# Optimization experiments

Hardware: AMD Instinct MI355X
Metric: run time of the kernel (lower is better)

Reference implementation:

```python
import jax, jax.numpy as jnp
import numpy as np
import math

HEADS = 16
D_MODEL = 1024
D_K = D_MODEL // HEADS


def setup_inputs() -> dict:
    key = jax.random.key(0)
    ks = jax.random.split(key, 11)
    B, S = 2, 2048
    s = 1.0 / math.sqrt(D_MODEL)
    return {
        "q": jax.random.normal(ks[0], (B, S, D_MODEL), jnp.float32),
        "k": jax.random.normal(ks[1], (B, S, D_MODEL), jnp.float32),
        "v": jax.random.normal(ks[2], (B, S, D_MODEL), jnp.float32),
        "Wq": jax.random.normal(ks[3], (D_MODEL, D_MODEL), jnp.float32) * s,
        "bq": jax.random.normal(ks[4], (D_MODEL,), jnp.float32) * s,
        "Wk": jax.random.normal(ks[5], (D_MODEL, D_MODEL), jnp.float32) * s,
        "bk": jax.random.normal(ks[6], (D_MODEL,), jnp.float32) * s,
        "Wv": jax.random.normal(ks[7], (D_MODEL, D_MODEL), jnp.float32) * s,
        "bv": jax.random.normal(ks[8], (D_MODEL,), jnp.float32) * s,
        "Wo": jax.random.normal(ks[9], (D_MODEL, D_MODEL), jnp.float32) * s,
        "bo": jax.random.normal(ks[10], (D_MODEL,), jnp.float32) * s,
    }


def reference(q, k, v, Wq, bq, Wk, bk, Wv, bv, Wo, bo):
    B, S, _ = q.shape
    # linear projections, split heads: [B, H, S, d_k]
    def proj(x, W, b):
        y = x @ W.T + b
        return y.reshape(B, -1, HEADS, D_K).transpose(0, 2, 1, 3)
    qh, kh, vh = proj(q, Wq, bq), proj(k, Wk, bk), proj(v, Wv, bv)
    # abs-modified scaled dot-product attention (no mask, eval -> no dropout)
    scores = jnp.abs(jnp.einsum("bhsd,bhtd->bhst", qh, kh) / math.sqrt(D_K))
    attn = jax.nn.softmax(scores, axis=-1)
    out = jnp.einsum("bhst,bhtd->bhsd", attn, vh)
    concat = out.transpose(0, 2, 1, 3).reshape(B, S, D_MODEL)
    return concat @ Wo.T + bo
```

## Files before the change

kernel.cpp:

```cpp
#include <hip/hip_runtime.h>

#define HEADS 16
#define DK 64
#define DM 1024
#define SEQ 2048
#define BATCH 2

using bf16x8 = __attribute__((ext_vector_type(8))) short;
using short4v = __attribute__((ext_vector_type(4))) short;
using f32x4 = __attribute__((ext_vector_type(4))) float;

static __device__ __forceinline__ short f2bf(float x) {
  union { float f; unsigned u; } c;
  c.f = x;
  unsigned r = (c.u + 0x7FFFu + ((c.u >> 16) & 1u)) >> 16;
  return (short)r;
}

static __device__ __forceinline__ void gload_lds16(const void* g, void* l) {
  __builtin_amdgcn_global_load_lds(
      (const __attribute__((address_space(1))) void*)g,
      (__attribute__((address_space(3))) void*)l, 16, 0, 0);
}

__global__ __launch_bounds__(256) void cvt7(
    const float* __restrict__ s0, const float* __restrict__ s1,
    const float* __restrict__ s2, const float* __restrict__ s3,
    const float* __restrict__ s4, const float* __restrict__ s5,
    const float* __restrict__ s6, short* d0, short* d1, short* d2, short* d3,
    short* d4, short* d5, short* d6) {
  const int y = blockIdx.y;
  const float* s;
  short* d;
  int n;
  switch (y) {
    case 0: s = s0; d = d0; n = BATCH * SEQ * DM; break;
    case 1: s = s1; d = d1; n = BATCH * SEQ * DM; break;
    case 2: s = s2; d = d2; n = BATCH * SEQ * DM; break;
    case 3: s = s3; d = d3; n = DM * DM; break;
    case 4: s = s4; d = d4; n = DM * DM; break;
    case 5: s = s5; d = d5; n = DM * DM; break;
    default: s = s6; d = d6; n = DM * DM; break;
  }
  const int n4 = n >> 2;
  const int stride = gridDim.x * 256;
  for (int i = blockIdx.x * 256 + threadIdx.x; i < n4; i += stride) {
    float4 v = ((const float4*)s)[i];
    short4v o;
    o.x = f2bf(v.x);
    o.y = f2bf(v.y);
    o.z = f2bf(v.z);
    o.w = f2bf(v.w);
    ((short4v*)d)[i] = o;
  }
}

__global__ __launch_bounds__(256) void proj_qkv(
    const short* __restrict__ Aq, const short* __restrict__ Ak,
    const short* __restrict__ Av, const short* __restrict__ Wq_,
    const short* __restrict__ Wk_, const short* __restrict__ Wv_,
    const float* __restrict__ bq, const float* __restrict__ bk,
    const float* __restrict__ bv, short* __restrict__ Qh,
    short* __restrict__ Kh, short* __restrict__ Vt) {
  __shared__ short smem[128 * 136];
  short* As = smem;
  short* Ws = smem + 8192;

  const int z = blockIdx.z;
  const short* A = z == 0 ? Aq : z == 1 ? Ak : Av;
  const short* W = z == 0 ? Wq_ : z == 1 ? Wk_ : Wv_;
  const float* bias = z == 0 ? bq : z == 1 ? bk : bv;
  short* C = z == 0 ? Qh : z == 1 ? Kh : Vt;
  const bool tr = (z == 2);

  const int tid = threadIdx.x;
  const int wave = tid >> 6, lane = tid & 63;
  const int quad = lane >> 4, l15 = lane & 15;
  const int n0 = blockIdx.x * 128, m0 = blockIdx.y * 128;
  const int mh = (wave & 1) * 64, nh = (wave >> 1) * 64;
  const int ldr = lane >> 3, ldc = lane & 7;

  f32x4 acc[4][4] = {};

  for (int k0 = 0; k0 < 1024; k0 += 64) {
    __syncthreads();
#pragma unroll
    for (int i = 0; i < 8; ++i) {
      int seg = wave * 8 + i;
      int r = (seg & 15) * 8 + ldr;
      int kb = ldc ^ (r & 7);
      if (seg < 16)
        gload_lds16(&A[(size_t)(m0 + r) * 1024 + k0 + kb * 8], &As[seg * 512]);
      else
        gload_lds16(&W[(size_t)(n0 + r) * 1024 + k0 + kb * 8],
                    &Ws[(seg - 16) * 512]);
    }
    __syncthreads();
#pragma unroll
    for (int ks = 0; ks < 2; ++ks) {
      bf16x8 a[4], b[4];
      int kb = ks * 4 + quad;
#pragma unroll
      for (int f = 0; f < 4; ++f) {
        int rm = mh + f * 16 + l15;
        int rn = nh + f * 16 + l15;
        a[f] = *(const bf16x8*)&As[rm * 64 + (kb ^ (rm & 7)) * 8];
        b[f] = *(const bf16x8*)&Ws[rn * 64 + (kb ^ (rn & 7)) * 8];
      }
#pragma unroll
      for (int mf = 0; mf < 4; ++mf)
#pragma unroll
        for (int nf = 0; nf < 4; ++nf)
          acc[mf][nf] = __builtin_amdgcn_mfma_f32_16x16x32_bf16(
              a[mf], b[nf], acc[mf][nf], 0, 0, 0);
    }
  }

  float bvv[4];
#pragma unroll
  for (int nf = 0; nf < 4; ++nf) bvv[nf] = bias[n0 + nh + nf * 16 + l15];

  __syncthreads();
  short* Cb = smem;

  if (!tr) {
#pragma unroll
    for (int mf = 0; mf < 4; ++mf)
#pragma unroll
      for (int nf = 0; nf < 4; ++nf)
#pragma unroll
        for (int r = 0; r < 4; ++r)
          Cb[(mh + mf * 16 + quad * 4 + r) * 136 + nh + nf * 16 + l15] =
              f2bf(acc[mf][nf][r] + bvv[nf]);
    __syncthreads();
#pragma unroll
    for (int j = 0; j < 8; ++j) {
      int cid = tid + 256 * j;
      int row = cid >> 4, cb = cid & 15;
      bf16x8 v = *(const bf16x8*)&Cb[row * 136 + cb * 8];
      int m = m0 + row, n = n0 + cb * 8;
      int b = m >> 11, s = m & (SEQ - 1), h = n >> 6, d = n & 63;
      *(bf16x8*)&C[((size_t)(b * HEADS + h) * SEQ + s) * DK + d] = v;
    }
  } else {
#pragma unroll
    for (int mf = 0; mf < 4; ++mf)
#pragma unroll
      for (int nf = 0; nf < 4; ++nf) {
        short4v p;
        p.x = f2bf(acc[mf][nf][0] + bvv[nf]);
        p.y = f2bf(acc[mf][nf][1] + bvv[nf]);
        p.z = f2bf(acc[mf][nf][2] + bvv[nf]);
        p.w = f2bf(acc[mf][nf][3] + bvv[nf]);
        *(short4v*)&Cb[(nh + nf * 16 + l15) * 136 + mh + mf * 16 + quad * 4] =
            p;
      }
    __syncthreads();
#pragma unroll
    for (int j = 0; j < 8; ++j) {
      int cid = tid + 256 * j;
      int row = cid >> 4, cb = cid & 15;
      bf16x8 v = *(const bf16x8*)&Cb[row * 136 + cb * 8];
      int n = n0 + row, m = m0 + cb * 8;
      int b = m >> 11, s = m & (SEQ - 1), h = n >> 6, d = n & 63;
      *(bf16x8*)&C[((size_t)(b * HEADS + h) * DK + d) * SEQ + s] = v;
    }
  }
}

__global__ __launch_bounds__(256) void proj_out(const short* __restrict__ A,
                                                const short* __restrict__ W,
                                                const float* __restrict__ bias,
                                                float* __restrict__ C) {
  __shared__ short smem[128 * 136];
  short* As = smem;
  short* Ws = smem + 8192;

  const int tid = threadIdx.x;
  const int wave = tid >> 6, lane = tid & 63;
  const int quad = lane >> 4, l15 = lane & 15;
  const int n0 = blockIdx.x * 128, m0 = blockIdx.y * 128;
  const int mh = (wave & 1) * 64, nh = (wave >> 1) * 64;
  const int ldr = lane >> 3, ldc = lane & 7;

  f32x4 acc[4][4] = {};

  for (int k0 = 0; k0 < 1024; k0 += 64) {
    __syncthreads();
#pragma unroll
    for (int i = 0; i < 8; ++i) {
      int seg = wave * 8 + i;
      int r = (seg & 15) * 8 + ldr;
      int kb = ldc ^ (r & 7);
      if (seg < 16)
        gload_lds16(&A[(size_t)(m0 + r) * 1024 + k0 + kb * 8], &As[seg * 512]);
      else
        gload_lds16(&W[(size_t)(n0 + r) * 1024 + k0 + kb * 8],
                    &Ws[(seg - 16) * 512]);
    }
    __syncthreads();
#pragma unroll
    for (int ks = 0; ks < 2; ++ks) {
      bf16x8 a[4], b[4];
      int kb = ks * 4 + quad;
#pragma unroll
      for (int f = 0; f < 4; ++f) {
        int rm = mh + f * 16 + l15;
        int rn = nh + f * 16 + l15;
        a[f] = *(const bf16x8*)&As[rm * 64 + (kb ^ (rm & 7)) * 8];
        b[f] = *(const bf16x8*)&Ws[rn * 64 + (kb ^ (rn & 7)) * 8];
      }
#pragma unroll
      for (int mf = 0; mf < 4; ++mf)
#pragma unroll
        for (int nf = 0; nf < 4; ++nf)
          acc[mf][nf] = __builtin_amdgcn_mfma_f32_16x16x32_bf16(
              a[mf], b[nf], acc[mf][nf], 0, 0, 0);
    }
  }

  float bvv[4];
#pragma unroll
  for (int nf = 0; nf < 4; ++nf) bvv[nf] = bias[n0 + nh + nf * 16 + l15];
#pragma unroll
  for (int mf = 0; mf < 4; ++mf)
#pragma unroll
    for (int nf = 0; nf < 4; ++nf)
#pragma unroll
      for (int r = 0; r < 4; ++r)
        C[(size_t)(m0 + mh + mf * 16 + quad * 4 + r) * 1024 + n0 + nh +
          nf * 16 + l15] = acc[mf][nf][r] + bvv[nf];
}

__global__ __launch_bounds__(256) void attn_mfma(const short* __restrict__ Qh,
                                                 const short* __restrict__ Kh,
                                                 const short* __restrict__ VtG,
                                                 short* __restrict__ concat) {
  __shared__ short Ks[64 * 64];
  __shared__ short Vt[64 * 64];
  __shared__ short Ps[128 * 64];

  const int tid = threadIdx.x;
  const int wave = tid >> 6, lane = tid & 63;
  const int quad = lane >> 4, l15 = lane & 15;
  const int bh = blockIdx.y;
  const int q0 = blockIdx.x * 128;
  const size_t base = (size_t)bh * SEQ * DK;
  const int ldr = lane >> 3, ldc = lane & 7;

  bf16x8 qf[2][2];
#pragma unroll
  for (int mf = 0; mf < 2; ++mf)
#pragma unroll
    for (int ks = 0; ks < 2; ++ks)
      qf[mf][ks] =
          *(const bf16x8*)&Qh[base +
                              (size_t)(q0 + wave * 32 + mf * 16 + l15) * 64 +
                              ks * 32 + quad * 8];

  f32x4 O[2][4] = {};
  float lsum[2][4] = {};

  for (int kt = 0; kt < SEQ / 64; ++kt) {
    __syncthreads();
#pragma unroll
    for (int i = 0; i < 2; ++i) {
      int seg = wave * 2 + i;
      int row = seg * 8 + ldr;
      int kb = ldc ^ (row & 7);
      gload_lds16(&Kh[base + (size_t)(kt * 64 + row) * 64 + kb * 8],
                  &Ks[seg * 512]);
      gload_lds16(&VtG[base + (size_t)row * SEQ + kt * 64 + kb * 8],
                  &Vt[seg * 512]);
    }
    __syncthreads();

    f32x4 sf[2][4] = {};
#pragma unroll
    for (int ks = 0; ks < 2; ++ks) {
      bf16x8 bfr[4];
      int kb = ks * 4 + quad;
#pragma unroll
      for (int nf = 0; nf < 4; ++nf) {
        int n = nf * 16 + l15;
        bfr[nf] = *(const bf16x8*)&Ks[n * 64 + (kb ^ (n & 7)) * 8];
      }
#pragma unroll
      for (int mf = 0; mf < 2; ++mf)
#pragma unroll
        for (int nf = 0; nf < 4; ++nf)
          sf[mf][nf] = __builtin_amdgcn_mfma_f32_16x16x32_bf16(
              qf[mf][ks], bfr[nf], sf[mf][nf], 0, 0, 0);
    }

    const int h2 = l15 >> 3, lo3 = l15 & 7;
#pragma unroll
    for (int mf = 0; mf < 2; ++mf)
#pragma unroll
      for (int nf = 0; nf < 4; ++nf) {
        const int ch = 2 * nf + h2;
#pragma unroll
        for (int r = 0; r < 4; ++r) {
          float e = __expf(fabsf(sf[mf][nf][r]) * 0.125f);
          lsum[mf][r] += e;
          int row = wave * 32 + mf * 16 + quad * 4 + r;
          Ps[(row << 6) + ((ch ^ ((row >> 1) & 7)) << 3) + lo3] = f2bf(e);
        }
      }
    __threadfence_block();

#pragma unroll
    for (int ks = 0; ks < 2; ++ks) {
      bf16x8 av[2], bvv[4];
      int kb = ks * 4 + quad;
#pragma unroll
      for (int mf = 0; mf < 2; ++mf) {
        int row = wave * 32 + mf * 16 + l15;
        av[mf] = *(const bf16x8*)&Ps[(row << 6) +
                                     ((kb ^ ((row >> 1) & 7)) << 3)];
      }
#pragma unroll
      for (int nf = 0; nf < 4; ++nf) {
        int n = nf * 16 + l15;
        bvv[nf] = *(const bf16x8*)&Vt[n * 64 + (kb ^ (n & 7)) * 8];
      }
#pragma unroll
      for (int mf = 0; mf < 2; ++mf)
#pragma unroll
        for (int nf = 0; nf < 4; ++nf)
          O[mf][nf] = __builtin_amdgcn_mfma_f32_16x16x32_bf16(
              av[mf], bvv[nf], O[mf][nf], 0, 0, 0);
    }
  }

  float inv[2][4];
#pragma unroll
  for (int mf = 0; mf < 2; ++mf)
#pragma unroll
    for (int r = 0; r < 4; ++r) {
      float s = lsum[mf][r];
#pragma unroll
      for (int x = 1; x < 16; x <<= 1) s += __shfl_xor(s, x, 64);
      inv[mf][r] = 1.f / s;
    }

  __syncthreads();
  const int h2 = l15 >> 3, lo3 = l15 & 7;
#pragma unroll
  for (int mf = 0; mf < 2; ++mf)
#pragma unroll
    for (int nf = 0; nf < 4; ++nf) {
      const int ch = 2 * nf + h2;
#pragma unroll
      for (int r = 0; r < 4; ++r) {
        int row = wave * 32 + mf * 16 + quad * 4 + r;
        Ps[(row << 6) + ((ch ^ ((row >> 1) & 7)) << 3) + lo3] =
            f2bf(O[mf][nf][r] * inv[mf][r]);
      }
    }
  __syncthreads();
  const int b = bh >> 4, h = bh & 15;
#pragma unroll
  for (int j = 0; j < 4; ++j) {
    int cid = tid + 256 * j;
    int row = cid >> 3, cb = cid & 7;
    bf16x8 v = *(const bf16x8*)&Ps[(row << 6) + ((cb ^ ((row >> 1) & 7)) << 3)];
    *(bf16x8*)&concat[((size_t)(b * SEQ + q0 + row)) * DM + h * 64 + cb * 8] =
        v;
  }
}

extern "C" void kernel_launch(void* const* d_in, const int* in_sizes, int n_in,
                              void* d_out, int out_size, void* d_ws,
                              size_t ws_size, hipStream_t stream) {
  const float* q = (const float*)d_in[0];
  const float* k = (const float*)d_in[1];
  const float* v = (const float*)d_in[2];
  const float* Wq = (const float*)d_in[3];
  const float* bq = (const float*)d_in[4];
  const float* Wk = (const float*)d_in[5];
  const float* bk = (const float*)d_in[6];
  const float* Wv = (const float*)d_in[7];
  const float* bv = (const float*)d_in[8];
  const float* Wo = (const float*)d_in[9];
  const float* bo = (const float*)d_in[10];

  short* ws = (short*)d_ws;
  const size_t T4 = (size_t)BATCH * SEQ * DM;
  const size_t T1 = (size_t)DM * DM;
  short* qb = ws;
  short* kb_ = ws + T4;
  short* vb = ws + 2 * T4;
  short* Wqb = ws + 3 * T4;
  short* Wkb = Wqb + T1;
  short* Wvb = Wqb + 2 * T1;
  short* Wob = Wqb + 3 * T1;
  short* Qh = Wqb + 4 * T1;
  short* Kh = Qh + T4;
  short* VtG = Qh + 2 * T4;
  short* cc = Qh + 3 * T4;

  cvt7<<<dim3(1024, 7), 256, 0, stream>>>(q, k, v, Wq, Wk, Wv, Wo, qb, kb_, vb,
                                          Wqb, Wkb, Wvb, Wob);

  proj_qkv<<<dim3(DM / 128, (BATCH * SEQ) / 128, 3), 256, 0, stream>>>(
      qb, kb_, vb, Wqb, Wkb, Wvb, bq, bk, bv, Qh, Kh, VtG);

  attn_mfma<<<dim3(SEQ / 128, BATCH * HEADS), 256, 0, stream>>>(Qh, Kh, VtG,
                                                                cc);

  proj_out<<<dim3(DM / 128, (BATCH * SEQ) / 128), 256, 0, stream>>>(
      cc, Wob, bo, (float*)d_out);
}
```

Measured before the change: 244.6 us.

## Double-buffer K/V tiles, fold softmax scale into Q, compute row sums via MFMA

The attention kernel now prefetches the next K/V tile into a second LDS buffer while computing on the current one, which removes one barrier per iteration. It shrinks the query tile to 64 rows (one 16-row fragment per wave), doubling the grid size. The scores are computed transposed (K as the A operand), so each lane writes packed 4-element P rows. The 1/sqrt(d_k)*log2(e) scale is folded into the Q projection epilogue, so the loop can use exp2 directly. Row sums come from an extra MFMA against a ones vector instead of per-element adds and a final shuffle reduction, at the cost of more MFMA work per tile and less Q reuse of each loaded K/V tile.

```diff
diff --git a/kernel.cpp b/kernel.cpp
--- a/kernel.cpp
+++ b/kernel.cpp
@@ -124,6 +124,7 @@
   short* Cb = smem;
 
   if (!tr) {
+    const float osc = (z == 0) ? 0.18033688011112042f : 1.0f;
 #pragma unroll
     for (int mf = 0; mf < 4; ++mf)
 #pragma unroll
@@ -131,7 +132,7 @@
 #pragma unroll
         for (int r = 0; r < 4; ++r)
           Cb[(mh + mf * 16 + quad * 4 + r) * 136 + nh + nf * 16 + l15] =
-              f2bf(acc[mf][nf][r] + bvv[nf]);
+              f2bf((acc[mf][nf][r] + bvv[nf]) * osc);
     __syncthreads();
 #pragma unroll
     for (int j = 0; j < 8; ++j) {
@@ -236,136 +237,128 @@
                                                  const short* __restrict__ Kh,
                                                  const short* __restrict__ VtG,
                                                  short* __restrict__ concat) {
-  __shared__ short Ks[64 * 64];
-  __shared__ short Vt[64 * 64];
-  __shared__ short Ps[128 * 64];
+  __shared__ short Ksm[2][64 * 64];
+  __shared__ short Vsm[2][64 * 64];
+  __shared__ short Ps[64 * 64];
 
   const int tid = threadIdx.x;
   const int wave = tid >> 6, lane = tid & 63;
   const int quad = lane >> 4, l15 = lane & 15;
   const int bh = blockIdx.y;
-  const int q0 = blockIdx.x * 128;
+  const int q0 = blockIdx.x * 64;
   const size_t base = (size_t)bh * SEQ * DK;
   const int ldr = lane >> 3, ldc = lane & 7;
-
-  bf16x8 qf[2][2];
-#pragma unroll
-  for (int mf = 0; mf < 2; ++mf)
-#pragma unroll
-    for (int ks = 0; ks < 2; ++ks)
-      qf[mf][ks] =
-          *(const bf16x8*)&Qh[base +
-                              (size_t)(q0 + wave * 32 + mf * 16 + l15) * 64 +
-                              ks * 32 + quad * 8];
-
-  f32x4 O[2][4] = {};
-  float lsum[2][4] = {};
-
+  const int row = wave * 16 + l15;
+  const int rsw = (row & 7) << 1;
+
+  bf16x8 qf[2];
+#pragma unroll
+  for (int ks = 0; ks < 2; ++ks)
+    qf[ks] =
+        *(const bf16x8*)&Qh[base + (size_t)(q0 + row) * 64 + ks * 32 + quad * 8];
+
+  bf16x8 ones;
+#pragma unroll
+  for (int i = 0; i < 8; ++i) ones[i] = (short)0x3F80;
+
+  f32x4 O[4] = {};
+  f32x4 Lacc = {};
+
+#pragma unroll
+  for (int i = 0; i < 2; ++i) {
+    int seg = wave * 2 + i;
+    int r = seg * 8 + ldr;
+    int kb = ldc ^ (r & 7);
+    gload_lds16(&Kh[base + (size_t)r * 64 + kb * 8], &Ksm[0][seg * 512]);
+    gload_lds16(&VtG[base + (size_t)r * SEQ + kb * 8], &Vsm[0][seg * 512]);
+  }
+  __syncthreads();
+
+  int cur = 0;
   for (int kt = 0; kt < SEQ / 64; ++kt) {
-    __syncthreads();
-#pragma unroll
-    for (int i = 0; i < 2; ++i) {
-      int seg = wave * 2 + i;
-      int row = seg * 8 + ldr;
-      int kb = ldc ^ (row & 7);
-      gload_lds16(&Kh[base + (size_t)(kt * 64 + row) * 64 + kb * 8],
-                  &Ks[seg * 512]);
-      gload_lds16(&VtG[base + (size_t)row * SEQ + kt * 64 + kb * 8],
-                  &Vt[seg * 512]);
-    }
-    __syncthreads();
-
-    f32x4 sf[2][4] = {};
+    if (kt + 1 < SEQ / 64) {
+#pragma unroll
+      for (int i = 0; i < 2; ++i) {
+        int seg = wave * 2 + i;
+        int r = seg * 8 + ldr;
+        int kb = ldc ^ (r & 7);
+        gload_lds16(&Kh[base + (size_t)((kt + 1) * 64 + r) * 64 + kb * 8],
+                    &Ksm[cur ^ 1][seg * 512]);
+        gload_lds16(&VtG[base + (size_t)r * SEQ + (kt + 1) * 64 + kb * 8],
+                    &Vsm[cur ^ 1][seg * 512]);
+      }
+    }
+
+    f32x4 sf[4] = {};
 #pragma unroll
     for (int ks = 0; ks < 2; ++ks) {
-      bf16x8 bfr[4];
+      bf16x8 kfr[4];
       int kb = ks * 4 + quad;
+#pragma unroll
+      for (int kf = 0; kf < 4; ++kf) {
+        int n = kf * 16 + l15;
+        kfr[kf] = *(const bf16x8*)&Ksm[cur][n * 64 + ((kb ^ (n & 7)) << 3)];
+      }
+#pragma unroll
+      for (int kf = 0; kf < 4; ++kf)
+        sf[kf] = __builtin_amdgcn_mfma_f32_16x16x32_bf16(kfr[kf], qf[ks],
+                                                         sf[kf], 0, 0, 0);
+    }
+
+#pragma unroll
+    for (int kf = 0; kf < 4; ++kf) {
+      short4v p;
+#pragma unroll
+      for (int r = 0; r < 4; ++r)
+        p[r] = f2bf(__builtin_amdgcn_exp2f(fabsf(sf[kf][r])));
+      *(short4v*)&Ps[row * 64 + (((kf * 4 + quad) ^ rsw) << 2)] = p;
+    }
+    __threadfence_block();
+
+#pragma unroll
+    for (int ks = 0; ks < 2; ++ks) {
+      int kb = ks * 4 + quad;
+      bf16x8 av =
+          *(const bf16x8*)&Ps[row * 64 + (((ks * 8 + quad * 2) ^ rsw) << 2)];
+      bf16x8 bv[4];
 #pragma unroll
       for (int nf = 0; nf < 4; ++nf) {
         int n = nf * 16 + l15;
-        bfr[nf] = *(const bf16x8*)&Ks[n * 64 + (kb ^ (n & 7)) * 8];
-      }
-#pragma unroll
-      for (int mf = 0; mf < 2; ++mf)
-#pragma unroll
-        for (int nf = 0; nf < 4; ++nf)
-          sf[mf][nf] = __builtin_amdgcn_mfma_f32_16x16x32_bf16(
-              qf[mf][ks], bfr[nf], sf[mf][nf], 0, 0, 0);
-    }
-
-    const int h2 = l15 >> 3, lo3 = l15 & 7;
-#pragma unroll
-    for (int mf = 0; mf < 2; ++mf)
-#pragma unroll
-      for (int nf = 0; nf < 4; ++nf) {
-        const int ch = 2 * nf + h2;
-#pragma unroll
-        for (int r = 0; r < 4; ++r) {
-          float e = __expf(fabsf(sf[mf][nf][r]) * 0.125f);
-          lsum[mf][r] += e;
-          int row = wave * 32 + mf * 16 + quad * 4 + r;
-          Ps[(row << 6) + ((ch ^ ((row >> 1) & 7)) << 3) + lo3] = f2bf(e);
-        }
-      }
-    __threadfence_block();
-
-#pragma unroll
-    for (int ks = 0; ks < 2; ++ks) {
-      bf16x8 av[2], bvv[4];
-      int kb = ks * 4 + quad;
-#pragma unroll
-      for (int mf = 0; mf < 2; ++mf) {
-        int row = wave * 32 + mf * 16 + l15;
-        av[mf] = *(const bf16x8*)&Ps[(row << 6) +
-                                     ((kb ^ ((row >> 1) & 7)) << 3)];
-      }
-#pragma unroll
-      for (int nf = 0; nf < 4; ++nf) {
-        int n = nf * 16 + l15;
-        bvv[nf] = *(const bf16x8*)&Vt[n * 64 + (kb ^ (n & 7)) * 8];
-      }
-#pragma unroll
-      for (int mf = 0; mf < 2; ++mf)
-#pragma unroll
-        for (int nf = 0; nf < 4; ++nf)
-          O[mf][nf] = __builtin_amdgcn_mfma_f32_16x16x32_bf16(
-              av[mf], bvv[nf], O[mf][nf], 0, 0, 0);
-    }
-  }
-
-  float inv[2][4];
-#pragma unroll
-  for (int mf = 0; mf < 2; ++mf)
+        bv[nf] = *(const bf16x8*)&Vsm[cur][n * 64 + ((kb ^ (n & 7)) << 3)];
+      }
+#pragma unroll
+      for (int nf = 0; nf < 4; ++nf)
+        O[nf] =
+            __builtin_amdgcn_mfma_f32_16x16x32_bf16(av, bv[nf], O[nf], 0, 0, 0);
+      Lacc = __builtin_amdgcn_mfma_f32_16x16x32_bf16(av, ones, Lacc, 0, 0, 0);
+    }
+
+    __syncthreads();
+    cur ^= 1;
+  }
+
+  float inv[4];
+#pragma unroll
+  for (int r = 0; r < 4; ++r) inv[r] = 1.f / Lacc[r];
+
+#pragma unroll
+  for (int nf = 0; nf < 4; ++nf)
 #pragma unroll
     for (int r = 0; r < 4; ++r) {
-      float s = lsum[mf][r];
-#pragma unroll
-      for (int x = 1; x < 16; x <<= 1) s += __shfl_xor(s, x, 64);
-      inv[mf][r] = 1.f / s;
-    }
-
-  __syncthreads();
-  const int h2 = l15 >> 3, lo3 = l15 & 7;
-#pragma unroll
-  for (int mf = 0; mf < 2; ++mf)
-#pragma unroll
-    for (int nf = 0; nf < 4; ++nf) {
-      const int ch = 2 * nf + h2;
-#pragma unroll
-      for (int r = 0; r < 4; ++r) {
-        int row = wave * 32 + mf * 16 + quad * 4 + r;
-        Ps[(row << 6) + ((ch ^ ((row >> 1) & 7)) << 3) + lo3] =
-            f2bf(O[mf][nf][r] * inv[mf][r]);
-      }
+      int rw = wave * 16 + quad * 4 + r;
+      int c8 = nf * 4 + (l15 >> 2);
+      Ps[rw * 64 + ((c8 ^ ((rw & 7) << 1)) << 2) + (l15 & 3)] =
+          f2bf(O[nf][r] * inv[r]);
     }
   __syncthreads();
   const int b = bh >> 4, h = bh & 15;
 #pragma unroll
-  for (int j = 0; j < 4; ++j) {
+  for (int j = 0; j < 2; ++j) {
     int cid = tid + 256 * j;
-    int row = cid >> 3, cb = cid & 7;
-    bf16x8 v = *(const bf16x8*)&Ps[(row << 6) + ((cb ^ ((row >> 1) & 7)) << 3)];
-    *(bf16x8*)&concat[((size_t)(b * SEQ + q0 + row)) * DM + h * 64 + cb * 8] =
+    int rrow = cid >> 3, cb = cid & 7;
+    bf16x8 v =
+        *(const bf16x8*)&Ps[rrow * 64 + (((cb * 2) ^ ((rrow & 7) << 1)) << 2)];
+    *(bf16x8*)&concat[((size_t)(b * SEQ + q0 + rrow)) * DM + h * 64 + cb * 8] =
         v;
   }
 }
@@ -406,8 +399,8 @@
   proj_qkv<<<dim3(DM / 128, (BATCH * SEQ) / 128, 3), 256, 0, stream>>>(
       qb, kb_, vb, Wqb, Wkb, Wvb, bq, bk, bv, Qh, Kh, VtG);
 
-  attn_mfma<<<dim3(SEQ / 128, BATCH * HEADS), 256, 0, stream>>>(Qh, Kh, VtG,
-                                                                cc);
+  attn_mfma<<<dim3(SEQ / 64, BATCH * HEADS), 256, 0, stream>>>(Qh, Kh, VtG,
+                                                               cc);
 
   proj_out<<<dim3(DM / 128, (BATCH * SEQ) / 128), 256, 0, stream>>>(
       cc, Wob, bo, (float*)d_out);
```

Result: no change. 240.3 us (-1.8%).

## Double-buffer K/V tiles, fold softmax scale into Q, MFMA row sums

Applied to the files above, without the earlier changes.

The attention kernel now double-buffers K and V tiles in LDS, so the global-to-LDS load for the next tile is issued while the current tile is computed, and only one barrier per iteration remains. The 1/sqrt(d_k)*log2(e) factor is folded into the Q projection epilogue, letting the inner loop use exp2 directly. The score MFMA is transposed (K as A operand) so each lane writes packed 4-element P vectors. Row sums are accumulated with an extra MFMA against a ones vector instead of scalar adds and shuffles. The cost is twice the LDS for K/V, which may lower occupancy, and row sums are now taken over bf16-rounded P values.

```diff
diff --git a/kernel.cpp b/kernel.cpp
--- a/kernel.cpp
+++ b/kernel.cpp
@@ -124,6 +124,7 @@
   short* Cb = smem;
 
   if (!tr) {
+    const float osc = (z == 0) ? 0.18033688011112042f : 1.0f;
 #pragma unroll
     for (int mf = 0; mf < 4; ++mf)
 #pragma unroll
@@ -131,7 +132,7 @@
 #pragma unroll
         for (int r = 0; r < 4; ++r)
           Cb[(mh + mf * 16 + quad * 4 + r) * 136 + nh + nf * 16 + l15] =
-              f2bf(acc[mf][nf][r] + bvv[nf]);
+              f2bf((acc[mf][nf][r] + bvv[nf]) * osc);
     __syncthreads();
 #pragma unroll
     for (int j = 0; j < 8; ++j) {
@@ -236,8 +237,8 @@
                                                  const short* __restrict__ Kh,
                                                  const short* __restrict__ VtG,
                                                  short* __restrict__ concat) {
-  __shared__ short Ks[64 * 64];
-  __shared__ short Vt[64 * 64];
+  __shared__ short Ksm[2][64 * 64];
+  __shared__ short Vsm[2][64 * 64];
   __shared__ short Ps[128 * 64];
 
   const int tid = threadIdx.x;
@@ -247,6 +248,9 @@
   const int q0 = blockIdx.x * 128;
   const size_t base = (size_t)bh * SEQ * DK;
   const int ldr = lane >> 3, ldc = lane & 7;
+  const int NT = SEQ / 64;
+  const int row0 = wave * 32 + l15;
+  const int rsw = (l15 & 7) << 1;
 
   bf16x8 qf[2][2];
 #pragma unroll
@@ -258,115 +262,121 @@
                               (size_t)(q0 + wave * 32 + mf * 16 + l15) * 64 +
                               ks * 32 + quad * 8];
 
+  bf16x8 ones;
+#pragma unroll
+  for (int i = 0; i < 8; ++i) ones[i] = (short)0x3F80;
+
   f32x4 O[2][4] = {};
-  float lsum[2][4] = {};
-
-  for (int kt = 0; kt < SEQ / 64; ++kt) {
-    __syncthreads();
+  f32x4 Lacc[2] = {};
+
+  auto stage = [&](int kt, int buf) {
 #pragma unroll
     for (int i = 0; i < 2; ++i) {
       int seg = wave * 2 + i;
-      int row = seg * 8 + ldr;
-      int kb = ldc ^ (row & 7);
-      gload_lds16(&Kh[base + (size_t)(kt * 64 + row) * 64 + kb * 8],
-                  &Ks[seg * 512]);
-      gload_lds16(&VtG[base + (size_t)row * SEQ + kt * 64 + kb * 8],
-                  &Vt[seg * 512]);
-    }
-    __syncthreads();
+      int r = seg * 8 + ldr;
+      int kb = ldc ^ (r & 7);
+      gload_lds16(&Kh[base + (size_t)(kt * 64 + r) * 64 + kb * 8],
+                  &Ksm[buf][seg * 512]);
+      gload_lds16(&VtG[base + (size_t)r * SEQ + kt * 64 + kb * 8],
+                  &Vsm[buf][seg * 512]);
+    }
+  };
+
+  stage(0, 0);
+  __syncthreads();
+
+  int cur = 0;
+  for (int kt = 0; kt < NT; ++kt) {
+    if (kt + 1 < NT) stage(kt + 1, cur ^ 1);
+
+    const short* Ks = Ksm[cur];
+    const short* Vs = Vsm[cur];
 
     f32x4 sf[2][4] = {};
 #pragma unroll
     for (int ks = 0; ks < 2; ++ks) {
-      bf16x8 bfr[4];
+      bf16x8 kfr[4];
       int kb = ks * 4 + quad;
 #pragma unroll
+      for (int kf = 0; kf < 4; ++kf) {
+        int n = kf * 16 + l15;
+        kfr[kf] = *(const bf16x8*)&Ks[n * 64 + ((kb ^ (n & 7)) << 3)];
+      }
+#pragma unroll
+      for (int kf = 0; kf < 4; ++kf)
+#pragma unroll
+        for (int mf = 0; mf < 2; ++mf)
+          sf[mf][kf] = __builtin_amdgcn_mfma_f32_16x16x32_bf16(
+              kfr[kf], qf[mf][ks], sf[mf][kf], 0, 0, 0);
+    }
+
+#pragma unroll
+    for (int mf = 0; mf < 2; ++mf)
+#pragma unroll
+      for (int kf = 0; kf < 4; ++kf) {
+        short4v p;
+#pragma unroll
+        for (int r = 0; r < 4; ++r)
+          p[r] = f2bf(__builtin_amdgcn_exp2f(fabsf(sf[mf][kf][r])));
+        *(short4v*)&Ps[(row0 + mf * 16) * 64 + (((kf * 4 + quad) ^ rsw) << 2)] =
+            p;
+      }
+    __threadfence_block();
+
+#pragma unroll
+    for (int ks = 0; ks < 2; ++ks) {
+      int kb = ks * 4 + quad;
+      bf16x8 av[2];
+#pragma unroll
+      for (int mf = 0; mf < 2; ++mf)
+        av[mf] = *(const bf16x8*)&Ps[(row0 + mf * 16) * 64 +
+                                     (((ks * 8 + quad * 2) ^ rsw) << 2)];
+      bf16x8 bvf[4];
+#pragma unroll
       for (int nf = 0; nf < 4; ++nf) {
-        int n = nf * 16 + l15;
-        bfr[nf] = *(const bf16x8*)&Ks[n * 64 + (kb ^ (n & 7)) * 8];
-      }
-#pragma unroll
-      for (int mf = 0; mf < 2; ++mf)
-#pragma unroll
-        for (int nf = 0; nf < 4; ++nf)
-          sf[mf][nf] = __builtin_amdgcn_mfma_f32_16x16x32_bf16(
-              qf[mf][ks], bfr[nf], sf[mf][nf], 0, 0, 0);
-    }
-
-    const int h2 = l15 >> 3, lo3 = l15 & 7;
-#pragma unroll
-    for (int mf = 0; mf < 2; ++mf)
-#pragma unroll
-      for (int nf = 0; nf < 4; ++nf) {
-        const int ch = 2 * nf + h2;
-#pragma unroll
-        for (int r = 0; r < 4; ++r) {
-          float e = __expf(fabsf(sf[mf][nf][r]) * 0.125f);
-          lsum[mf][r] += e;
-          int row = wave * 32 + mf * 16 + quad * 4 + r;
-          Ps[(row << 6) + ((ch ^ ((row >> 1) & 7)) << 3) + lo3] = f2bf(e);
-        }
-      }
-    __threadfence_block();
-
-#pragma unroll
-    for (int ks = 0; ks < 2; ++ks) {
-      bf16x8 av[2], bvv[4];
-      int kb = ks * 4 + quad;
+        int d = nf * 16 + l15;
+        bvf[nf] = *(const bf16x8*)&Vs[d * 64 + ((kb ^ (d & 7)) << 3)];
+      }
 #pragma unroll
       for (int mf = 0; mf < 2; ++mf) {
-        int row = wave * 32 + mf * 16 + l15;
-        av[mf] = *(const bf16x8*)&Ps[(row << 6) +
-                                     ((kb ^ ((row >> 1) & 7)) << 3)];
-      }
-#pragma unroll
-      for (int nf = 0; nf < 4; ++nf) {
-        int n = nf * 16 + l15;
-        bvv[nf] = *(const bf16x8*)&Vt[n * 64 + (kb ^ (n & 7)) * 8];
-      }
-#pragma unroll
-      for (int mf = 0; mf < 2; ++mf)
 #pragma unroll
         for (int nf = 0; nf < 4; ++nf)
           O[mf][nf] = __builtin_amdgcn_mfma_f32_16x16x32_bf16(
-              av[mf], bvv[nf], O[mf][nf], 0, 0, 0);
-    }
-  }
-
-  float inv[2][4];
+              av[mf], bvf[nf], O[mf][nf], 0, 0, 0);
+        Lacc[mf] = __builtin_amdgcn_mfma_f32_16x16x32_bf16(av[mf], ones,
+                                                           Lacc[mf], 0, 0, 0);
+      }
+    }
+
+    __syncthreads();
+    cur ^= 1;
+  }
+
+  float inv_[2][4];
 #pragma unroll
   for (int mf = 0; mf < 2; ++mf)
 #pragma unroll
-    for (int r = 0; r < 4; ++r) {
-      float s = lsum[mf][r];
-#pragma unroll
-      for (int x = 1; x < 16; x <<= 1) s += __shfl_xor(s, x, 64);
-      inv[mf][r] = 1.f / s;
-    }
-
-  __syncthreads();
-  const int h2 = l15 >> 3, lo3 = l15 & 7;
+    for (int r = 0; r < 4; ++r) inv_[mf][r] = 1.f / Lacc[mf][r];
+
 #pragma unroll
   for (int mf = 0; mf < 2; ++mf)
 #pragma unroll
-    for (int nf = 0; nf < 4; ++nf) {
-      const int ch = 2 * nf + h2;
+    for (int nf = 0; nf < 4; ++nf)
 #pragma unroll
       for (int r = 0; r < 4; ++r) {
-        int row = wave * 32 + mf * 16 + quad * 4 + r;
-        Ps[(row << 6) + ((ch ^ ((row >> 1) & 7)) << 3) + lo3] =
-            f2bf(O[mf][nf][r] * inv[mf][r]);
-      }
-    }
+        int rw = wave * 32 + mf * 16 + quad * 4 + r;
+        int d = nf * 16 + l15;
+        Ps[rw * 64 + (((d >> 3) ^ (rw & 7)) << 3) + (d & 7)] =
+            f2bf(O[mf][nf][r] * inv_[mf][r]);
+      }
   __syncthreads();
   const int b = bh >> 4, h = bh & 15;
 #pragma unroll
   for (int j = 0; j < 4; ++j) {
     int cid = tid + 256 * j;
-    int row = cid >> 3, cb = cid & 7;
-    bf16x8 v = *(const bf16x8*)&Ps[(row << 6) + ((cb ^ ((row >> 1) & 7)) << 3)];
-    *(bf16x8*)&concat[((size_t)(b * SEQ + q0 + row)) * DM + h * 64 + cb * 8] =
-        v;
+    int rw = cid >> 3, g = cid & 7;
+    bf16x8 v = *(const bf16x8*)&Ps[rw * 64 + ((g ^ (rw & 7)) << 3)];
+    *(bf16x8*)&concat[((size_t)(b * SEQ + q0 + rw)) * DM + h * 64 + g * 8] = v;
   }
 }
 
```

Result: faster. 238.0 us (-2.7%).
